# Performance work log

Hardware: AMD Instinct MI355X
Metric: run time of the kernel (lower is better)

Reference implementation:

```python
import jax, jax.numpy as jnp
import numpy as np

GROUPS = 32
EPS = 1e-6


def group_norm(x, gamma, beta):
    # x: [B, C, T], normalize per group of channels over (C//G, T)
    B, C, T = x.shape
    xr = x.reshape(B, GROUPS, C // GROUPS, T)
    mean = xr.mean(axis=(2, 3), keepdims=True)
    var = xr.var(axis=(2, 3), keepdims=True)
    xn = ((xr - mean) * jax.lax.rsqrt(var + EPS)).reshape(B, C, T)
    return xn * gamma[None, :, None] + beta[None, :, None]


def conv1x1(h, w, b):
    # 1x1 Conv1d == channel matmul. h: [B,C,T], w: [O,C], b: [O]
    return jnp.einsum('oc,bct->bot', w, h) + b[None, :, None]


def setup_inputs() -> dict:
    key = jax.random.key(0)
    ks = jax.random.split(key, 10)
    B, C, T = 8, 512, 2048
    s = 1.0 / np.sqrt(C)
    return {
        'x': jax.random.normal(ks[0], (B, C, T), jnp.float32),
        'gamma': jnp.ones((C,), jnp.float32),
        'beta': jnp.zeros((C,), jnp.float32),
        'q_w': jax.random.normal(ks[1], (C, C), jnp.float32) * s,
        'q_b': jnp.zeros((C,), jnp.float32),
        'k_w': jax.random.normal(ks[2], (C, C), jnp.float32) * s,
        'k_b': jnp.zeros((C,), jnp.float32),
        'v_w': jax.random.normal(ks[3], (C, C), jnp.float32) * s,
        'v_b': jnp.zeros((C,), jnp.float32),
        'o_w': jax.random.normal(ks[4], (C, C), jnp.float32) * s,
        'o_b': jnp.zeros((C,), jnp.float32),
    }


def reference(x, gamma, beta, q_w, q_b, k_w, k_b, v_w, v_b, o_w, o_b):
    h = group_norm(x, gamma, beta)
    q = conv1x1(h, q_w, q_b)  # [B,C,T]
    k = conv1x1(h, k_w, k_b)
    v = conv1x1(h, v_w, v_b)
    B, C, T = q.shape
    scale = jnp.asarray(C, q.dtype) ** -0.5
    # scores[b,t,s] = sum_c q[b,c,t] * k[b,c,s]
    scores = jnp.einsum('bct,bcs->bts', q, k) * scale
    w = jax.nn.softmax(scores, axis=-1)
    # out[b,c,t] = sum_s v[b,c,s] * w[b,t,s]
    h = jnp.einsum('bcs,bts->bct', v, w)
    h = conv1x1(h, o_w, o_b)
    return x + h
```

## Files before the change

kernel.cpp:

```cpp
#include <hip/hip_runtime.h>
#include <hip/hip_bf16.h>
#include <stdint.h>

typedef __bf16 bf16_t;
typedef __attribute__((ext_vector_type(8))) __bf16 bf16x8;
typedef __attribute__((ext_vector_type(4))) __bf16 bf16x4;
typedef __attribute__((ext_vector_type(4))) float f32x4;

__device__ __forceinline__ bool is_fp32(const void* gamma) {
  return ((const unsigned*)gamma)[0] == 0x3F800000u;
}

__device__ __forceinline__ void async_copy16(const bf16_t* g, bf16_t* l) {
  __builtin_amdgcn_global_load_lds(
      (const __attribute__((address_space(1))) void*)g,
      (__attribute__((address_space(3))) void*)l, 16, 0, 0);
}

#define GFENCE() asm volatile("" ::: "memory")

__device__ __forceinline__ void hard_barrier() {
  GFENCE();
  __builtin_amdgcn_sched_barrier(0);
  __builtin_amdgcn_s_barrier();
  __builtin_amdgcn_sched_barrier(0);
  GFENCE();
}

template <int NW>
__device__ __forceinline__ void vm_wait() {
  if constexpr (NW == 8)
    asm volatile("s_waitcnt vmcnt(8)" ::: "memory");
  else if constexpr (NW == 6)
    asm volatile("s_waitcnt vmcnt(6)" ::: "memory");
  else
    asm volatile("s_waitcnt vmcnt(0)" ::: "memory");
}

__global__ __launch_bounds__(512) void gnorm(
    const void* __restrict__ xv, const void* __restrict__ gamma,
    const void* __restrict__ beta, const void* __restrict__ q_w,
    const void* __restrict__ k_w, const void* __restrict__ v_w,
    const void* __restrict__ o_w, const void* __restrict__ q_b,
    const void* __restrict__ k_b, const void* __restrict__ v_b,
    const void* __restrict__ o_b, bf16_t* __restrict__ wdst,
    float* __restrict__ rowsum, bf16_t* __restrict__ ht) {
  const bool fp32 = is_fp32(gamma);
  const int bid = blockIdx.x;
  const int tid = threadIdx.x;
  if (bid < 64) {
    const void* wsrc[4] = {q_w, k_w, v_w, o_w};
#pragma unroll
    for (int r = 0; r < 4; ++r) {
      int e = (bid * 2048 + r * 512 + tid) * 8;
      int seg = e >> 18, off = e & 262143;
      const void* s = wsrc[seg];
      bf16x8 w8;
      if (fp32) {
        const float* sf = (const float*)s + off;
        float4 u = *(const float4*)sf;
        float4 w = *(const float4*)(sf + 4);
        w8[0] = (bf16_t)u.x; w8[1] = (bf16_t)u.y;
        w8[2] = (bf16_t)u.z; w8[3] = (bf16_t)u.w;
        w8[4] = (bf16_t)w.x; w8[5] = (bf16_t)w.y;
        w8[6] = (bf16_t)w.z; w8[7] = (bf16_t)w.w;
      } else {
        w8 = *(const bf16x8*)((const bf16_t*)s + off);
      }
      *(bf16x8*)(wdst + e) = w8;
    }
    if (bid == 0) {
      bf16_t* vdst = wdst + 4 * 262144;
      const void* vsrc[6] = {gamma, beta, q_b, k_b, v_b, o_b};
#pragma unroll
      for (int rep = 0; rep < 6; ++rep) {
        const void* s2 = vsrc[rep];
        vdst[rep * 512 + tid] = fp32 ? (bf16_t)((const float*)s2)[tid]
                                     : ((const bf16_t*)s2)[tid];
      }
    }
    if (bid >= 1 && bid <= 8) {
      float4 z = {0.f, 0.f, 0.f, 0.f};
      *(float4*)(rowsum + (((bid - 1) << 9) + tid) * 4) = z;
    }
    return;
  }
  __shared__ float tile[16 * 2052];
  __shared__ float red[16];
  const int gn = bid - 64;
  const int b = gn >> 5, g = gn & 31;
  const long long base = ((long long)b * 512 + g * 16) * 2048;
  float s1 = 0.f, s2 = 0.f;
  if (fp32) {
    const float* xf = (const float*)xv + base;
#pragma unroll
    for (int p = 0; p < 16; ++p) {
      float4 u = *(const float4*)(xf + p * 2048 + tid * 4);
      s1 += u.x + u.y + u.z + u.w;
      s2 += u.x * u.x + u.y * u.y + u.z * u.z + u.w * u.w;
      *(float4*)&tile[p * 2052 + tid * 4] = u;
    }
  } else {
    const bf16_t* xb = (const bf16_t*)xv + base;
#pragma unroll
    for (int p = 0; p < 16; ++p) {
      bf16x4 v4 = *(const bf16x4*)(xb + p * 2048 + tid * 4);
      float4 u;
      u.x = (float)v4[0]; u.y = (float)v4[1];
      u.z = (float)v4[2]; u.w = (float)v4[3];
      s1 += u.x + u.y + u.z + u.w;
      s2 += u.x * u.x + u.y * u.y + u.z * u.z + u.w * u.w;
      *(float4*)&tile[p * 2052 + tid * 4] = u;
    }
  }
  for (int o = 32; o > 0; o >>= 1) {
    s1 += __shfl_down(s1, o);
    s2 += __shfl_down(s2, o);
  }
  const int wv = tid >> 6, ln = tid & 63;
  if (ln == 0) { red[wv] = s1; red[8 + wv] = s2; }
  __syncthreads();
  float a = 0.f, c2 = 0.f;
#pragma unroll
  for (int w = 0; w < 8; ++w) { a += red[w]; c2 += red[8 + w]; }
  const float inv = 1.0f / 32768.0f;
  float mean = a * inv;
  float var = c2 * inv - mean * mean;
  float rstd = rsqrtf(var + 1e-6f);

  const int c = ln & 15;
  const int tq = ln >> 4;
  const int gc = g * 16 + c;
  float gamv = fp32 ? ((const float*)gamma)[gc]
                    : (float)((const bf16_t*)gamma)[gc];
  float betv = fp32 ? ((const float*)beta)[gc]
                    : (float)((const bf16_t*)beta)[gc];
  float sc = rstd * gamv;
  float sh = betv - mean * sc;
  bf16_t* hb = ht + (long long)b * 2048 * 512 + g * 16;
#pragma unroll 4
  for (int pass = 0; pass < 64; ++pass) {
    int t = wv * 256 + pass * 4 + tq;
    float v = tile[c * 2052 + t];
    hb[(long long)t * 512 + c] = (bf16_t)(v * sc + sh);
  }
}

template <int BM, bool BIASM, bool BIASN, bool RESOUT, bool EXPSUM,
          bool NORMROW, int M, int N, int K, int LDA, int LDB, int LDC>
__device__ __forceinline__ void gemm8_body(
    const bf16_t* __restrict__ A, long long sA, const bf16_t* __restrict__ B,
    long long sB, void* __restrict__ Cout, long long sC,
    const bf16_t* __restrict__ biasM, const bf16_t* __restrict__ biasN,
    const void* __restrict__ Res, long long sR, float alpha,
    const void* __restrict__ gamma, float* __restrict__ rowsum, int m0,
    int n0, int b, bf16_t* lds) {
  static_assert(!RESOUT || BM == 128, "RESOUT epilogue assumes BM=128");
  constexpr int AI = BM / 32;
  constexpr int AR = BM * 32;
  constexpr int L = BM / 128 + 2;
  const int tid = threadIdx.x;
  const int lane = tid & 63;
  const int lane15 = lane & 15;
  const int quad = lane >> 4;
  const int wave = tid >> 6;
  const int wm = wave >> 2;
  const int wn = wave & 3;

  bf16_t* ldsA = lds;
  bf16_t* ldsB = lds + 4 * AR;

  const int srow = tid >> 2;
  const int sg = ((tid & 3) - (srow >> 1)) & 3;
  const long long A128 = 128LL * LDA, B128 = 128LL * LDB;
  const bf16_t* As_src = A + (long long)b * sA + (long long)m0 * LDA +
                         (long long)srow * LDA + sg * 8;
  const bf16_t* Bs_src = B + (long long)b * sB + (long long)n0 * LDB +
                         (long long)srow * LDB + sg * 8;

  auto stA = [&](int kelem, int r) {
    async_copy16(As_src + kelem, ldsA + r * AR + tid * 8);
    if constexpr (BM == 256)
      async_copy16(As_src + A128 + kelem, ldsA + r * AR + tid * 8 + 4096);
  };
  auto stB = [&](int kelem, int r) {
    async_copy16(Bs_src + kelem, ldsB + r * 8192 + tid * 8);
    async_copy16(Bs_src + B128 + kelem, ldsB + r * 8192 + tid * 8 + 4096);
  };

  const int slot = ((quad + (lane15 >> 1)) & 3) * 8;
  const int aoff = (wm * (BM / 2) + lane15) * 32 + slot;
  const int boff = (wn * 64 + lane15) * 32 + slot;

  bf16x8 af[AI];
  f32x4 acc[AI][4];
#pragma unroll
  for (int i = 0; i < AI; ++i)
#pragma unroll
    for (int j = 0; j < 4; ++j) acc[i][j] = {0.f, 0.f, 0.f, 0.f};

  auto lda_frags = [&](int r) {
#pragma unroll
    for (int i = 0; i < AI; ++i)
      af[i] = *(const bf16x8*)(ldsA + r * AR + aoff + i * 512);
  };
  auto ldbf = [&](int r, int j) {
    return *(const bf16x8*)(ldsB + r * 8192 + boff + j * 512);
  };

  auto phaseA = [&](int rdA, int rdB, int stk, int str) {
    lda_frags(rdA);
    bf16x8 b0 = ldbf(rdB, 0), b1 = ldbf(rdB, 1);
    stA(stk, str);
    hard_barrier();
    asm volatile("s_waitcnt lgkmcnt(0)" ::: "memory");
    __builtin_amdgcn_sched_barrier(0);
    __builtin_amdgcn_s_setprio(1);
#pragma unroll
    for (int i = 0; i < AI; ++i) {
      acc[i][0] = __builtin_amdgcn_mfma_f32_16x16x32_bf16(af[i], b0, acc[i][0], 0, 0, 0);
      acc[i][1] = __builtin_amdgcn_mfma_f32_16x16x32_bf16(af[i], b1, acc[i][1], 0, 0, 0);
    }
    __builtin_amdgcn_s_setprio(0);
    hard_barrier();
  };
  auto phaseB = [&](int rdB, int stk, int str) {
    bf16x8 b0 = ldbf(rdB, 2), b1 = ldbf(rdB, 3);
    stB(stk, str);
    hard_barrier();
    asm volatile("s_waitcnt lgkmcnt(0)" ::: "memory");
    __builtin_amdgcn_sched_barrier(0);
    __builtin_amdgcn_s_setprio(1);
#pragma unroll
    for (int i = 0; i < AI; ++i) {
      acc[i][2] = __builtin_amdgcn_mfma_f32_16x16x32_bf16(af[i], b0, acc[i][2], 0, 0, 0);
      acc[i][3] = __builtin_amdgcn_mfma_f32_16x16x32_bf16(af[i], b1, acc[i][3], 0, 0, 0);
    }
    __builtin_amdgcn_s_setprio(0);
    vm_wait<2 * L>();
    hard_barrier();
  };

  constexpr int NI = K / 128;

  stA(0, 0); stB(0, 0);
  stA(32, 1); stB(32, 1);
  stA(64, 2); stB(64, 2);
  vm_wait<2 * L>();
  hard_barrier();

#pragma unroll 1
  for (int it = 0; it < NI; ++it) {
    const int ku = it * 128;
    const bool lastit = (it == NI - 1);
    const int k0n = lastit ? 0 : ku + 128;
    const int k1n = lastit ? 32 : ku + 160;
    const int k2n = lastit ? 64 : ku + 192;
    phaseA(0, 0, ku + 96, 3);
    phaseB(0, ku + 96, 3);
    phaseA(1, 1, k0n, 0);
    phaseB(1, k0n, 0);
    phaseA(2, 2, k1n, 1);
    phaseB(2, k1n, 1);
    phaseA(3, 3, k2n, 2);
    phaseB(3, k2n, 2);
  }
  asm volatile("s_waitcnt vmcnt(0)" ::: "memory");
  hard_barrier();

  if constexpr (EXPSUM) {
    bf16_t* ebuf = lds;
#pragma unroll
    for (int i = 0; i < AI; ++i) {
#pragma unroll
      for (int r = 0; r < 4; ++r) {
        int ml = wm * (BM / 2) + i * 16 + quad * 4 + r;
        float partial = 0.f;
#pragma unroll
        for (int j = 0; j < 4; ++j) {
          int nl = wn * 64 + j * 16 + lane15;
          float v = __expf(acc[i][j][r] * alpha);
          partial += v;
          ebuf[(ml * 256 + nl) ^ ((ml & 7) << 3)] = (bf16_t)v;
        }
        partial += __shfl_xor(partial, 1);
        partial += __shfl_xor(partial, 2);
        partial += __shfl_xor(partial, 4);
        partial += __shfl_xor(partial, 8);
        if (lane15 == 0)
          atomicAdd(&rowsum[(long long)b * M + m0 + ml], partial);
      }
    }
    __syncthreads();
    bf16_t* Co = (bf16_t*)Cout + (long long)b * sC;
#pragma unroll
    for (int p = 0; p < BM / 16; ++p) {
      int v8 = tid + p * 512;
      int mr = v8 >> 5, c8 = v8 & 31;
      bf16x8 w = *(const bf16x8*)&ebuf[(mr * 256 + c8 * 8) ^ ((mr & 7) << 3)];
      *(bf16x8*)&Co[(long long)(m0 + mr) * LDC + n0 + c8 * 8] = w;
    }
    return;
  }

  if constexpr (RESOUT) {
    float* fbuf = (float*)lds;
#pragma unroll
    for (int i = 0; i < AI; ++i) {
#pragma unroll
      for (int j = 0; j < 4; ++j) {
#pragma unroll
        for (int r = 0; r < 4; ++r) {
          int ml = wm * (BM / 2) + i * 16 + quad * 4 + r;
          int nl = wn * 64 + j * 16 + lane15;
          float v = acc[i][j][r] * alpha;
          if constexpr (BIASM) v += (float)biasM[m0 + ml];
          if constexpr (BIASN) v += (float)biasN[n0 + nl];
          fbuf[(ml * 256 + nl) ^ ((ml & 7) << 2)] = v;
        }
      }
    }
    __syncthreads();
    const bool f32o = is_fp32(gamma);
#pragma unroll
    for (int p = 0; p < BM / 8; ++p) {
      int v4 = tid + p * 512;
      int mr = v4 >> 6, c4 = v4 & 63;
      float4 w = *(const float4*)&fbuf[(mr * 256 + c4 * 4) ^ ((mr & 7) << 2)];
      long long base = (long long)(m0 + mr) * LDC + n0 + c4 * 4;
      if (f32o) {
        float4 xr = *(const float4*)((const float*)Res + (long long)b * sR + base);
        w.x += xr.x; w.y += xr.y; w.z += xr.z; w.w += xr.w;
        *(float4*)&((float*)Cout)[(long long)b * sC + base] = w;
      } else {
        bf16x4 xr = *(const bf16x4*)((const bf16_t*)Res + (long long)b * sR + base);
        bf16x4 o4;
        o4[0] = (bf16_t)(w.x + (float)xr[0]);
        o4[1] = (bf16_t)(w.y + (float)xr[1]);
        o4[2] = (bf16_t)(w.z + (float)xr[2]);
        o4[3] = (bf16_t)(w.w + (float)xr[3]);
        *(bf16x4*)&((bf16_t*)Cout)[(long long)b * sC + base] = o4;
      }
    }
    return;
  }

  {
    float invr[AI][4];
    if constexpr (NORMROW) {
#pragma unroll
      for (int i = 0; i < AI; ++i)
#pragma unroll
        for (int r = 0; r < 4; ++r)
          invr[i][r] = 1.0f / rowsum[(long long)b * M + m0 + wm * (BM / 2) +
                                     i * 16 + quad * 4 + r];
    }
    bf16_t* ebuf = lds;
#pragma unroll
    for (int i = 0; i < AI; ++i) {
#pragma unroll
      for (int j = 0; j < 4; ++j) {
#pragma unroll
        for (int r = 0; r < 4; ++r) {
          int ml = wm * (BM / 2) + i * 16 + quad * 4 + r;
          int nl = wn * 64 + j * 16 + lane15;
          float v = acc[i][j][r] * alpha;
          if constexpr (NORMROW) v *= invr[i][r];
          if constexpr (BIASM) v += (float)biasM[m0 + ml];
          if constexpr (BIASN) v += (float)biasN[n0 + nl];
          ebuf[(ml * 256 + nl) ^ ((ml & 7) << 3)] = (bf16_t)v;
        }
      }
    }
    __syncthreads();
    bf16_t* Co = (bf16_t*)Cout + (long long)b * sC;
#pragma unroll
    for (int p = 0; p < BM / 16; ++p) {
      int v8 = tid + p * 512;
      int mr = v8 >> 5, c8 = v8 & 31;
      bf16x8 w = *(const bf16x8*)&ebuf[(mr * 256 + c8 * 8) ^ ((mr & 7) << 3)];
      *(bf16x8*)&Co[(long long)(m0 + mr) * LDC + n0 + c8 * 8] = w;
    }
  }
}

__global__ __launch_bounds__(512, 2) void qkv_fat(
    const bf16_t* __restrict__ ht, const bf16_t* __restrict__ wdst,
    bf16_t* __restrict__ qkt, bf16_t* __restrict__ vvb,
    const void* __restrict__ gamma) {
  __shared__ __align__(16) bf16_t lds[65536];
  const long long TC = 2048LL * 512, CT = 512LL * 2048;
  const bf16_t* vdst = wdst + 4 * 262144;
  const bf16_t* qkb = vdst + 1024;
  const bf16_t* vbb = vdst + 2048;
  const bf16_t* wv = wdst + 2 * 262144;
  int bid = blockIdx.x;
  if (bid < 256) {
    int b = bid >> 5, rem = bid & 31;
    int m0 = (rem >> 2) * 256, n0 = (rem & 3) * 256;
    gemm8_body<256, false, true, false, false, false, 2048, 1024, 512, 512,
               512, 1024>(ht, TC, wdst, 0, qkt, 2048LL * 1024, nullptr, qkb,
                          nullptr, 0, 1.0f, gamma, nullptr, m0, n0, b, lds);
  } else {
    int id2 = bid - 256;
    int b = id2 >> 5, rem = id2 & 31;
    int m0 = (rem & 3) * 128, n0 = (rem >> 2) * 256;
    gemm8_body<128, true, false, false, false, false, 512, 2048, 512, 512,
               512, 2048>(wv, 0, ht, TC, vvb, CT, vbb, nullptr, nullptr, 0,
                          1.0f, gamma, nullptr, m0, n0, b, lds);
  }
}

__global__ __launch_bounds__(512, 2) void scores_kernel(
    const bf16_t* __restrict__ qkt, bf16_t* __restrict__ Sm,
    const void* __restrict__ gamma, float* __restrict__ rowsum, float alpha) {
  __shared__ __align__(16) bf16_t lds[65536];
  int x = blockIdx.x;
  int gid = x >> 4, win = x & 15;
  int gm = gid & 1, gn = gid >> 1;
  int m0 = (gm * 4 + (win & 3)) * 256;
  int n0 = (gn * 4 + (win >> 2)) * 256;
  gemm8_body<256, false, false, false, true, false, 2048, 2048, 512, 1024,
             1024, 2048>(qkt, 2048LL * 1024, qkt + 512, 2048LL * 1024, Sm,
                         2048LL * 2048, nullptr, nullptr, nullptr, 0, alpha,
                         gamma, rowsum, m0, n0, blockIdx.z, lds);
}

__global__ __launch_bounds__(512, 2) void av_kernel(
    const bf16_t* __restrict__ Sm, const bf16_t* __restrict__ vvb,
    bf16_t* __restrict__ h2t, const void* __restrict__ gamma,
    float* __restrict__ rowsum) {
  __shared__ __align__(16) bf16_t lds[49152];
  gemm8_body<128, false, false, false, false, true, 2048, 512, 2048, 2048,
             2048, 512>(Sm, 2048LL * 2048, vvb, 512LL * 2048, h2t,
                        2048LL * 512, nullptr, nullptr, nullptr, 0, 1.0f,
                        gamma, rowsum, blockIdx.y * 128, blockIdx.x * 256,
                        blockIdx.z, lds);
}

__global__ __launch_bounds__(512, 2) void final_kernel(
    const bf16_t* __restrict__ wdst, const bf16_t* __restrict__ h2t,
    void* __restrict__ out, const void* __restrict__ x,
    const void* __restrict__ gamma) {
  __shared__ __align__(16) bf16_t lds[65536];
  const bf16_t* vdst = wdst + 4 * 262144;
  const bf16_t* obb = vdst + 2560;
  const bf16_t* wo = wdst + 3 * 262144;
  gemm8_body<128, true, false, true, false, false, 512, 2048, 512, 512, 512,
             2048>(wo, 0, h2t, 2048LL * 512, out, 512LL * 2048, obb, nullptr,
                   x, 512LL * 2048, 1.0f, gamma, nullptr, blockIdx.y * 128,
                   blockIdx.x * 256, blockIdx.z, lds);
}

extern "C" void kernel_launch(void* const* d_in, const int* in_sizes, int n_in,
                              void* d_out, int out_size, void* d_ws,
                              size_t ws_size, hipStream_t stream) {
  const void* x = d_in[0];
  const void* gamma = d_in[1];
  const void* beta = d_in[2];
  const void* q_w = d_in[3];
  const void* q_b = d_in[4];
  const void* k_w = d_in[5];
  const void* k_b = d_in[6];
  const void* v_w = d_in[7];
  const void* v_b = d_in[8];
  const void* o_w = d_in[9];
  const void* o_b = d_in[10];

  const long long BTC = 8LL * 2048 * 512;
  char* ws = (char*)d_ws;
  bf16_t* wdst = (bf16_t*)(ws + 4096);
  float* rowsum = (float*)(ws + 4096 + 2 * 1024 * 1024 + 8192);
  const size_t hdr = 4096 + 2 * 1024 * 1024 + 8192 + 65536;
  bf16_t* ht = (bf16_t*)(ws + hdr);
  bf16_t* vvb = ht + BTC;
  bf16_t* Sm = vvb + BTC;
  bf16_t* qkt = (bf16_t*)d_out;

  const float scale = 0.044194173824159216f;

  gnorm<<<320, 512, 0, stream>>>(x, gamma, beta, q_w, k_w, v_w, o_w, q_b, k_b,
                                 v_b, o_b, wdst, rowsum, ht);
  qkv_fat<<<512, 512, 0, stream>>>(ht, wdst, qkt, vvb, gamma);
  scores_kernel<<<dim3(64, 1, 8), 512, 0, stream>>>(qkt, Sm, gamma, rowsum,
                                                    scale);
  av_kernel<<<dim3(2, 16, 8), 512, 0, stream>>>(Sm, vvb, ht, gamma, rowsum);
  final_kernel<<<dim3(8, 4, 8), 512, 0, stream>>>(wdst, ht, d_out, x, gamma);
}
```

Before: 276.1 us.

## Add 3-stage ring GEMM with 128x256 tiles for QKV and scores kernels

Introduces a new GEMM body with a 3-deep LDS ring buffer using async global-to-LDS copies and 32-wide k-steps, split into two MFMA phases per step. The QKV projection and scores kernels switch to 128x256 tiles with smaller LDS (36864 bf16), launch bounds raised to 4 blocks per CU, and twice as many blocks. The aim is higher occupancy and better load/compute overlap. The cost is more barriers per k-step and smaller tiles with less data reuse.

```diff
diff --git a/kernel.cpp b/kernel.cpp
--- a/kernel.cpp
+++ b/kernel.cpp
@@ -33,6 +33,8 @@
     asm volatile("s_waitcnt vmcnt(8)" ::: "memory");
   else if constexpr (NW == 6)
     asm volatile("s_waitcnt vmcnt(6)" ::: "memory");
+  else if constexpr (NW == 3)
+    asm volatile("s_waitcnt vmcnt(3)" ::: "memory");
   else
     asm volatile("s_waitcnt vmcnt(0)" ::: "memory");
 }
@@ -143,6 +145,153 @@
     int t = wv * 256 + pass * 4 + tq;
     float v = tile[c * 2052 + t];
     hb[(long long)t * 512 + c] = (bf16_t)(v * sc + sh);
+  }
+}
+
+template <bool BIASM, bool BIASN, bool EXPSUM, int M, int N, int K, int LDA,
+          int LDB, int LDC>
+__device__ __forceinline__ void gemm_ring3(
+    const bf16_t* __restrict__ A, long long sA, const bf16_t* __restrict__ B,
+    long long sB, bf16_t* __restrict__ Cout, long long sC,
+    const bf16_t* __restrict__ biasM, const bf16_t* __restrict__ biasN,
+    float alpha, float* __restrict__ rowsum, int m0, int n0, int b,
+    bf16_t* lds) {
+  const int tid = threadIdx.x;
+  const int lane = tid & 63;
+  const int lane15 = lane & 15;
+  const int quad = lane >> 4;
+  const int wave = tid >> 6;
+  const int wm = wave >> 2;
+  const int wn = wave & 3;
+
+  bf16_t* ldsA = lds;
+  bf16_t* ldsB = lds + 3 * 4096;
+
+  const int srow = tid >> 2;
+  const int sg = ((tid & 3) - (srow >> 1)) & 3;
+  const long long B128 = 128LL * LDB;
+  const bf16_t* As_src = A + (long long)b * sA + (long long)m0 * LDA +
+                         (long long)srow * LDA + sg * 8;
+  const bf16_t* Bs_src = B + (long long)b * sB + (long long)n0 * LDB +
+                         (long long)srow * LDB + sg * 8;
+
+  auto stA = [&](int kelem, int r) {
+    async_copy16(As_src + kelem, ldsA + r * 4096 + tid * 8);
+  };
+  auto stB = [&](int kelem, int r) {
+    async_copy16(Bs_src + kelem, ldsB + r * 8192 + tid * 8);
+    async_copy16(Bs_src + B128 + kelem, ldsB + r * 8192 + tid * 8 + 4096);
+  };
+
+  const int slot = ((quad + (lane15 >> 1)) & 3) * 8;
+  const int aoff = (wm * 64 + lane15) * 32 + slot;
+  const int boff = (wn * 64 + lane15) * 32 + slot;
+
+  bf16x8 af[4];
+  f32x4 acc[4][4];
+#pragma unroll
+  for (int i = 0; i < 4; ++i)
+#pragma unroll
+    for (int j = 0; j < 4; ++j) acc[i][j] = {0.f, 0.f, 0.f, 0.f};
+
+  auto ldbf = [&](int r, int j) {
+    return *(const bf16x8*)(ldsB + r * 8192 + boff + j * 512);
+  };
+
+  constexpr int NT = K / 32;
+
+  stA(0, 0); stB(0, 0);
+  stA(32, 1); stB(32, 1);
+  vm_wait<3>();
+  hard_barrier();
+
+#pragma unroll 1
+  for (int kt = 0; kt < NT; ++kt) {
+    const int rd = kt % 3;
+    const int rs = (kt + 2) % 3;
+    const int ks = ((kt + 2) % NT) * 32;
+#pragma unroll
+    for (int i = 0; i < 4; ++i)
+      af[i] = *(const bf16x8*)(ldsA + rd * 4096 + aoff + i * 512);
+    bf16x8 b0 = ldbf(rd, 0), b1 = ldbf(rd, 1);
+    stA(ks, rs);
+    hard_barrier();
+    asm volatile("s_waitcnt lgkmcnt(0)" ::: "memory");
+    __builtin_amdgcn_sched_barrier(0);
+    __builtin_amdgcn_s_setprio(1);
+#pragma unroll
+    for (int i = 0; i < 4; ++i) {
+      acc[i][0] = __builtin_amdgcn_mfma_f32_16x16x32_bf16(af[i], b0, acc[i][0], 0, 0, 0);
+      acc[i][1] = __builtin_amdgcn_mfma_f32_16x16x32_bf16(af[i], b1, acc[i][1], 0, 0, 0);
+    }
+    __builtin_amdgcn_s_setprio(0);
+    hard_barrier();
+    bf16x8 b2 = ldbf(rd, 2), b3 = ldbf(rd, 3);
+    stB(ks, rs);
+    hard_barrier();
+    asm volatile("s_waitcnt lgkmcnt(0)" ::: "memory");
+    __builtin_amdgcn_sched_barrier(0);
+    __builtin_amdgcn_s_setprio(1);
+#pragma unroll
+    for (int i = 0; i < 4; ++i) {
+      acc[i][2] = __builtin_amdgcn_mfma_f32_16x16x32_bf16(af[i], b2, acc[i][2], 0, 0, 0);
+      acc[i][3] = __builtin_amdgcn_mfma_f32_16x16x32_bf16(af[i], b3, acc[i][3], 0, 0, 0);
+    }
+    __builtin_amdgcn_s_setprio(0);
+    vm_wait<3>();
+    hard_barrier();
+  }
+  asm volatile("s_waitcnt vmcnt(0)" ::: "memory");
+  hard_barrier();
+
+  bf16_t* ebuf = lds;
+  if constexpr (EXPSUM) {
+#pragma unroll
+    for (int i = 0; i < 4; ++i) {
+#pragma unroll
+      for (int r = 0; r < 4; ++r) {
+        int ml = wm * 64 + i * 16 + quad * 4 + r;
+        float partial = 0.f;
+#pragma unroll
+        for (int j = 0; j < 4; ++j) {
+          int nl = wn * 64 + j * 16 + lane15;
+          float v = __expf(acc[i][j][r] * alpha);
+          partial += v;
+          ebuf[(ml * 256 + nl) ^ ((ml & 7) << 3)] = (bf16_t)v;
+        }
+        partial += __shfl_xor(partial, 1);
+        partial += __shfl_xor(partial, 2);
+        partial += __shfl_xor(partial, 4);
+        partial += __shfl_xor(partial, 8);
+        if (lane15 == 0)
+          atomicAdd(&rowsum[(long long)b * M + m0 + ml], partial);
+      }
+    }
+  } else {
+#pragma unroll
+    for (int i = 0; i < 4; ++i) {
+#pragma unroll
+      for (int j = 0; j < 4; ++j) {
+#pragma unroll
+        for (int r = 0; r < 4; ++r) {
+          int ml = wm * 64 + i * 16 + quad * 4 + r;
+          int nl = wn * 64 + j * 16 + lane15;
+          float v = acc[i][j][r] * alpha;
+          if constexpr (BIASM) v += (float)biasM[m0 + ml];
+          if constexpr (BIASN) v += (float)biasN[n0 + nl];
+          ebuf[(ml * 256 + nl) ^ ((ml & 7) << 3)] = (bf16_t)v;
+        }
+      }
+    }
+  }
+  __syncthreads();
+  bf16_t* Co = Cout + (long long)b * sC;
+#pragma unroll
+  for (int p = 0; p < 8; ++p) {
+    int v8 = tid + p * 512;
+    int mr = v8 >> 5, c8 = v8 & 31;
+    bf16x8 w = *(const bf16x8*)&ebuf[(mr * 256 + c8 * 8) ^ ((mr & 7) << 3)];
+    *(bf16x8*)&Co[(long long)(m0 + mr) * LDC + n0 + c8 * 8] = w;
   }
 }
 
@@ -268,41 +417,6 @@
   asm volatile("s_waitcnt vmcnt(0)" ::: "memory");
   hard_barrier();
 
-  if constexpr (EXPSUM) {
-    bf16_t* ebuf = lds;
-#pragma unroll
-    for (int i = 0; i < AI; ++i) {
-#pragma unroll
-      for (int r = 0; r < 4; ++r) {
-        int ml = wm * (BM / 2) + i * 16 + quad * 4 + r;
-        float partial = 0.f;
-#pragma unroll
-        for (int j = 0; j < 4; ++j) {
-          int nl = wn * 64 + j * 16 + lane15;
-          float v = __expf(acc[i][j][r] * alpha);
-          partial += v;
-          ebuf[(ml * 256 + nl) ^ ((ml & 7) << 3)] = (bf16_t)v;
-        }
-        partial += __shfl_xor(partial, 1);
-        partial += __shfl_xor(partial, 2);
-        partial += __shfl_xor(partial, 4);
-        partial += __shfl_xor(partial, 8);
-        if (lane15 == 0)
-          atomicAdd(&rowsum[(long long)b * M + m0 + ml], partial);
-      }
-    }
-    __syncthreads();
-    bf16_t* Co = (bf16_t*)Cout + (long long)b * sC;
-#pragma unroll
-    for (int p = 0; p < BM / 16; ++p) {
-      int v8 = tid + p * 512;
-      int mr = v8 >> 5, c8 = v8 & 31;
-      bf16x8 w = *(const bf16x8*)&ebuf[(mr * 256 + c8 * 8) ^ ((mr & 7) << 3)];
-      *(bf16x8*)&Co[(long long)(m0 + mr) * LDC + n0 + c8 * 8] = w;
-    }
-    return;
-  }
-
   if constexpr (RESOUT) {
     float* fbuf = (float*)lds;
 #pragma unroll
@@ -384,46 +498,44 @@
   }
 }
 
-__global__ __launch_bounds__(512, 2) void qkv_fat(
+__global__ __launch_bounds__(512, 4) void qkv_fat(
     const bf16_t* __restrict__ ht, const bf16_t* __restrict__ wdst,
     bf16_t* __restrict__ qkt, bf16_t* __restrict__ vvb,
     const void* __restrict__ gamma) {
-  __shared__ __align__(16) bf16_t lds[65536];
+  __shared__ __align__(16) bf16_t lds[36864];
   const long long TC = 2048LL * 512, CT = 512LL * 2048;
   const bf16_t* vdst = wdst + 4 * 262144;
   const bf16_t* qkb = vdst + 1024;
   const bf16_t* vbb = vdst + 2048;
   const bf16_t* wv = wdst + 2 * 262144;
   int bid = blockIdx.x;
-  if (bid < 256) {
-    int b = bid >> 5, rem = bid & 31;
-    int m0 = (rem >> 2) * 256, n0 = (rem & 3) * 256;
-    gemm8_body<256, false, true, false, false, false, 2048, 1024, 512, 512,
-               512, 1024>(ht, TC, wdst, 0, qkt, 2048LL * 1024, nullptr, qkb,
-                          nullptr, 0, 1.0f, gamma, nullptr, m0, n0, b, lds);
+  if (bid < 512) {
+    int b = bid >> 6, rem = bid & 63;
+    int m0 = (rem >> 2) * 128, n0 = (rem & 3) * 256;
+    gemm_ring3<false, true, false, 2048, 1024, 512, 512, 512, 1024>(
+        ht, TC, wdst, 0, qkt, 2048LL * 1024, nullptr, qkb, 1.0f, nullptr, m0,
+        n0, b, lds);
   } else {
-    int id2 = bid - 256;
+    int id2 = bid - 512;
     int b = id2 >> 5, rem = id2 & 31;
     int m0 = (rem & 3) * 128, n0 = (rem >> 2) * 256;
-    gemm8_body<128, true, false, false, false, false, 512, 2048, 512, 512,
-               512, 2048>(wv, 0, ht, TC, vvb, CT, vbb, nullptr, nullptr, 0,
-                          1.0f, gamma, nullptr, m0, n0, b, lds);
-  }
-}
-
-__global__ __launch_bounds__(512, 2) void scores_kernel(
+    gemm_ring3<true, false, false, 512, 2048, 512, 512, 512, 2048>(
+        wv, 0, ht, TC, vvb, CT, vbb, nullptr, 1.0f, nullptr, m0, n0, b, lds);
+  }
+}
+
+__global__ __launch_bounds__(512, 4) void scores_kernel(
     const bf16_t* __restrict__ qkt, bf16_t* __restrict__ Sm,
     const void* __restrict__ gamma, float* __restrict__ rowsum, float alpha) {
-  __shared__ __align__(16) bf16_t lds[65536];
+  __shared__ __align__(16) bf16_t lds[36864];
   int x = blockIdx.x;
   int gid = x >> 4, win = x & 15;
-  int gm = gid & 1, gn = gid >> 1;
-  int m0 = (gm * 4 + (win & 3)) * 256;
+  int gm = gid & 3, gn = gid >> 2;
+  int m0 = (gm * 4 + (win & 3)) * 128;
   int n0 = (gn * 4 + (win >> 2)) * 256;
-  gemm8_body<256, false, false, false, true, false, 2048, 2048, 512, 1024,
-             1024, 2048>(qkt, 2048LL * 1024, qkt + 512, 2048LL * 1024, Sm,
-                         2048LL * 2048, nullptr, nullptr, nullptr, 0, alpha,
-                         gamma, rowsum, m0, n0, blockIdx.z, lds);
+  gemm_ring3<false, false, true, 2048, 2048, 512, 1024, 1024, 2048>(
+      qkt, 2048LL * 1024, qkt + 512, 2048LL * 1024, Sm, 2048LL * 2048,
+      nullptr, nullptr, alpha, rowsum, m0, n0, blockIdx.z, lds);
 }
 
 __global__ __launch_bounds__(512, 2) void av_kernel(
@@ -481,9 +593,9 @@
 
   gnorm<<<320, 512, 0, stream>>>(x, gamma, beta, q_w, k_w, v_w, o_w, q_b, k_b,
                                  v_b, o_b, wdst, rowsum, ht);
-  qkv_fat<<<512, 512, 0, stream>>>(ht, wdst, qkt, vvb, gamma);
-  scores_kernel<<<dim3(64, 1, 8), 512, 0, stream>>>(qkt, Sm, gamma, rowsum,
-                                                    scale);
+  qkv_fat<<<768, 512, 0, stream>>>(ht, wdst, qkt, vvb, gamma);
+  scores_kernel<<<dim3(128, 1, 8), 512, 0, stream>>>(qkt, Sm, gamma, rowsum,
+                                                     scale);
   av_kernel<<<dim3(2, 16, 8), 512, 0, stream>>>(Sm, vvb, ht, gamma, rowsum);
   final_kernel<<<dim3(8, 4, 8), 512, 0, stream>>>(wdst, ht, d_out, x, gamma);
 }
```

Measured after the change: 266.9 us. 3.3% less time.
